# Kernel optimization log

Measured on AMD Instinct MI355X. Metric: run time of the kernel, lower is better.

The kernel has to match this reference:

```python
import jax, jax.numpy as jnp
import numpy as np

SEQ, BATCH, DIM = 2048, 32, 1024


def setup_inputs() -> dict:
    key = jax.random.key(0)
    k1, k2, k3, k4, k5 = jax.random.split(key, 5)
    scale = 1.0 / np.sqrt(DIM)
    return {
        "decoder_hidden": jax.random.normal(k1, (BATCH, 1, DIM), dtype=jnp.float32),
        "encoder_out": jax.random.normal(k2, (SEQ, BATCH, DIM), dtype=jnp.float32),
        "W_enc": jax.random.normal(k3, (DIM, DIM), dtype=jnp.float32) * scale,
        "W_dec": jax.random.normal(k4, (DIM, DIM), dtype=jnp.float32) * scale,
        "V_att": jax.random.normal(k5, (1, DIM), dtype=jnp.float32) * scale,
    }


def reference(decoder_hidden, encoder_out, W_enc, W_dec, V_att):
    # encoder_out: (seq, batch, dim); decoder_hidden: (batch, 1, dim)
    # torch Linear: y = x @ W.T with W of shape (out, in)
    keys = jnp.einsum('sbd,ed->bse', encoder_out, W_enc)      # (batch, seq, dim)
    query = decoder_hidden @ W_dec.T                           # (batch, 1, dim)
    scores = jnp.tanh(keys + query)                            # (batch, seq, dim)
    logits = jnp.einsum('bsd,d->bs', scores, V_att[0])         # (batch, seq)
    alpha = jax.nn.softmax(logits, axis=1)[..., None]          # (batch, seq, 1)
    # context = alpha^T @ encoder_out_permuted -> (batch, 1, dim)
    context = jnp.einsum('bs,sbd->bd', alpha[..., 0], encoder_out)[:, None, :]
    return context, jnp.transpose(alpha, (2, 0, 1))            # (1, batch, seq)
```

## Files before the change

### kernel.cpp

```cpp
#include <hip/hip_runtime.h>
#include <hip/hip_bf16.h>
#include <math.h>

#define SEQ   2048
#define BATCH 32
#define DIM   1024
#define MROWS (SEQ*BATCH)
#define NT2   4
#define NCH   16
#define NKT   32

typedef __attribute__((ext_vector_type(8))) short short8;
typedef __attribute__((ext_vector_type(8))) unsigned short u16x8;
typedef __attribute__((ext_vector_type(4))) float f32x4;

__device__ __forceinline__ unsigned short f2bf(float f) {
  unsigned u = __builtin_bit_cast(unsigned, f);
  u += 0x7FFFu + ((u >> 16) & 1u);
  return (unsigned short)(u >> 16);
}

__device__ __forceinline__ void gl16(const unsigned short* g, unsigned short* l) {
  __builtin_amdgcn_global_load_lds(
      (const __attribute__((address_space(1))) unsigned int*)g,
      (__attribute__((address_space(3))) unsigned int*)l, 16, 0, 0);
}

__global__ __launch_bounds__(256) void conv_bf16_k(const float* __restrict__ src,
                                                   unsigned short* __restrict__ dst) {
  size_t i = ((size_t)blockIdx.x * 256 + threadIdx.x) * 8;
  f32x4 a = __builtin_nontemporal_load(reinterpret_cast<const f32x4*>(src + i));
  f32x4 b = __builtin_nontemporal_load(reinterpret_cast<const f32x4*>(src + i + 4));
  u16x8 o;
  o[0] = f2bf(a[0]); o[1] = f2bf(a[1]); o[2] = f2bf(a[2]); o[3] = f2bf(a[3]);
  o[4] = f2bf(b[0]); o[5] = f2bf(b[1]); o[6] = f2bf(b[2]); o[7] = f2bf(b[3]);
  *reinterpret_cast<u16x8*>(dst + i) = o;
}

__global__ __launch_bounds__(256) void qpart_k(const float* __restrict__ dh,
                                               const float* __restrict__ Wd,
                                               float* __restrict__ qpart) {
  const int bx = blockIdx.x;
  const int eb = bx & 3;
  const int dc = bx >> 2;
  __shared__ float ldh[BATCH][128];
  const int tid = threadIdx.x;
#pragma unroll
  for (int i = 0; i < 4; ++i) {
    int idx = tid + i * 256;
    int bb = idx >> 5, d4 = idx & 31;
    float4 v = *reinterpret_cast<const float4*>(&dh[(size_t)bb * DIM + dc * 128 + d4 * 4]);
    *reinterpret_cast<float4*>(&ldh[bb][d4 * 4]) = v;
  }
  __syncthreads();
  const int e = eb * 256 + tid;
  float acc[BATCH];
#pragma unroll
  for (int b = 0; b < BATCH; ++b) acc[b] = 0.f;
  for (int d4 = 0; d4 < 32; ++d4) {
    float4 w = *reinterpret_cast<const float4*>(&Wd[(size_t)e * DIM + dc * 128 + d4 * 4]);
#pragma unroll
    for (int b = 0; b < BATCH; ++b) {
      float4 h = *reinterpret_cast<const float4*>(&ldh[b][d4 * 4]);
      acc[b] += w.x * h.x + w.y * h.y + w.z * h.z + w.w * h.w;
    }
  }
#pragma unroll
  for (int b = 0; b < BATCH; ++b)
    qpart[((size_t)dc * BATCH + b) * DIM + e] = acc[b];
}

__global__ __launch_bounds__(256) void qred_k(const float* __restrict__ qpart,
                                              float* __restrict__ q) {
  int i = blockIdx.x * 256 + threadIdx.x;
  float s = 0.f;
#pragma unroll
  for (int dc = 0; dc < 8; ++dc) s += qpart[(size_t)dc * 32768 + i];
  q[i] = s;
}

#define BARR  __builtin_amdgcn_s_barrier()
#define VMC(n) asm volatile("s_waitcnt vmcnt(" #n ")" ::: "memory")

#define STAGE_A(t, h) do {                                                        \
    gl16(Abase + (size_t)(gAr + (h) * 64) * 1024 + (t) * 32 + cSt * 8,            \
         (unsigned short*)(arena + (((t) & 1) * 32768) + (h) * 8192) + w * 512);  \
  } while (0)

#define STAGE_B(t, h) do {                                                        \
    gl16(Bbase + (size_t)(gBr + (h) * 32) * 1024 + (t) * 32 + cSt * 8,            \
         (unsigned short*)(arena + (((t) & 1) * 32768) + 16384 + (h) * 8192)      \
             + w * 512);                                                          \
  } while (0)

#define LOAD_A(d, MH) do {                                                        \
    const char* bA_ = arena + (d) * 32768 + (MH) * 8192;                          \
    _Pragma("unroll") for (int i_ = 0; i_ < 4; ++i_) {                            \
      int lrow_ = wr * 64 + i_ * 16 + fr;                                         \
      int lc_ = kq ^ ((lrow_ >> 1) & 3);                                          \
      a[i_] = *(const short8*)(bA_ + lrow_ * 64 + lc_ * 16);                      \
    } } while (0)

#define LOAD_B(SET, d, NH) do {                                                   \
    const char* bB_ = arena + (d) * 32768 + 16384 + (NH) * 8192;                  \
    _Pragma("unroll") for (int j_ = 0; j_ < 2; ++j_) {                            \
      int lrow_ = wc * 32 + j_ * 16 + fr;                                         \
      int lc_ = kq ^ ((lrow_ >> 1) & 3);                                          \
      SET[j_] = *(const short8*)(bB_ + lrow_ * 64 + lc_ * 16);                    \
    } } while (0)

#define QUAD(BSET, MH, NH) do {                                                   \
    __builtin_amdgcn_s_setprio(1);                                                \
    _Pragma("unroll") for (int i_ = 0; i_ < 4; ++i_)                              \
    _Pragma("unroll") for (int j_ = 0; j_ < 2; ++j_)                              \
      acc[(MH) * 4 + i_][(NH) * 2 + j_] =                                         \
          __builtin_amdgcn_mfma_f32_16x16x32_bf16(                                \
              a[i_], BSET[j_], acc[(MH) * 4 + i_][(NH) * 2 + j_], 0, 0, 0);       \
    __builtin_amdgcn_s_setprio(0);                                                \
  } while (0)

__global__ __launch_bounds__(512, 2) void gemm8p(const unsigned short* __restrict__ A,
                                                 const unsigned short* __restrict__ B,
                                                 const float* __restrict__ q,
                                                 const float* __restrict__ V,
                                                 float* __restrict__ lpart) {
  __shared__ __align__(16) char arena[65536];

  const int bid = blockIdx.x;
  const int wg = (bid & 7) * 128 + (bid >> 3);
  const int mt = wg >> 2, nt = wg & 3;
  const int row0 = mt * 256, col0 = nt * 256;
  const int tid = threadIdx.x;
  const int lane = tid & 63, w = tid >> 6;
  const int wr = w >> 2, wc = w & 3;
  const int fr = lane & 15, kq = lane >> 4;

  const int lr0 = tid >> 2;
  const int cSt = (tid & 3) ^ ((lr0 >> 1) & 3);
  const int gAr = (lr0 & 63) + (lr0 >> 6) * 128;
  const int gBr = (lr0 & 31) + (lr0 >> 5) * 64;

  const unsigned short* Abase = A + (size_t)row0 * DIM;
  const unsigned short* Bbase = B + (size_t)col0 * DIM;

  f32x4 acc[8][4];
#pragma unroll
  for (int i = 0; i < 8; ++i)
#pragma unroll
    for (int j = 0; j < 4; ++j) acc[i][j] = (f32x4)(0.f);

  short8 a[4];
  short8 b0[2], b1[2];

  STAGE_A(0, 0); STAGE_B(0, 0); STAGE_A(0, 1); STAGE_B(0, 1);
  STAGE_A(1, 0); STAGE_B(1, 0);
  VMC(2);
  BARR;

#pragma unroll 1
  for (int t2 = 0; t2 < NKT; t2 += 2) {
    const bool last = (t2 == NKT - 2);
    LOAD_A(0, 0); LOAD_B(b0, 0, 0); LOAD_B(b1, 0, 1);
    STAGE_A(t2 + 1, 1); STAGE_B(t2 + 1, 1);
    BARR; QUAD(b0, 0, 0); QUAD(b1, 0, 1); BARR;
    LOAD_A(0, 1);
    if (!last) { STAGE_A(t2 + 2, 0); STAGE_B(t2 + 2, 0); VMC(2); } else { VMC(0); }
    BARR; QUAD(b0, 1, 0); QUAD(b1, 1, 1); BARR;
    LOAD_A(1, 0); LOAD_B(b0, 1, 0); LOAD_B(b1, 1, 1);
    if (!last) { STAGE_A(t2 + 2, 1); STAGE_B(t2 + 2, 1); }
    BARR; QUAD(b0, 0, 0); QUAD(b1, 0, 1); BARR;
    LOAD_A(1, 1);
    if (!last) { STAGE_A(t2 + 3, 0); STAGE_B(t2 + 3, 0); VMC(2); }
    BARR; QUAD(b0, 1, 0); QUAD(b1, 1, 1); BARR;
  }

  __syncthreads();
  float* qld = (float*)arena;
  float* vld = (float*)(arena + 33280);
  float* red = (float*)(arena + 34304);
#pragma unroll
  for (int i = 0; i < 4; ++i) {
    int id = i * 512 + tid;
    int bb = id >> 6, e4 = id & 63;
    float4 v = *(const float4*)&q[(size_t)bb * DIM + col0 + e4 * 4];
    *(float4*)&qld[bb * 260 + e4 * 4] = v;
  }
  if (tid < 64) *(float4*)&vld[tid * 4] = *(const float4*)&V[col0 + tid * 4];
  __syncthreads();

#pragma unroll
  for (int mf = 0; mf < 8; ++mf) {
#pragma unroll
    for (int reg = 0; reg < 4; ++reg) {
      const int m_loc = wr * 128 + mf * 16 + kq * 4 + reg;
      const int bb = m_loc & 31;
      float val = 0.f;
#pragma unroll
      for (int nf = 0; nf < 4; ++nf) {
        const int el = wc * 64 + nf * 16 + fr;
        float x = acc[mf][nf][reg] + qld[bb * 260 + el];
        float g = __expf(2.f * x);
        float tnh = 1.f - 2.f * __builtin_amdgcn_rcpf(g + 1.f);
        val += tnh * vld[el];
      }
      val += __shfl_xor(val, 1); val += __shfl_xor(val, 2);
      val += __shfl_xor(val, 4); val += __shfl_xor(val, 8);
      if (fr == 0) red[wc * 256 + m_loc] = val;
    }
  }
  __syncthreads();
  if (tid < 256) {
    float s = red[tid] + red[256 + tid] + red[512 + tid] + red[768 + tid];
    lpart[(size_t)(row0 + tid) * NT2 + nt] = s;
  }
}

__global__ __launch_bounds__(256) void softmax_k(const float* __restrict__ lpart,
                                                 float* __restrict__ alpha) {
  const int b = blockIdx.x;
  __shared__ float lv[SEQ];
  __shared__ float sred[4];
  const int tid = threadIdx.x;
  float mx = -1e30f;
  for (int s = tid; s < SEQ; s += 256) {
    const float* p = &lpart[(size_t)(s * BATCH + b) * NT2];
    float v = p[0] + p[1] + p[2] + p[3];
    lv[s] = v;
    mx = fmaxf(mx, v);
  }
#pragma unroll
  for (int off = 32; off >= 1; off >>= 1) mx = fmaxf(mx, __shfl_xor(mx, off));
  if ((tid & 63) == 0) sred[tid >> 6] = mx;
  __syncthreads();
  mx = fmaxf(fmaxf(sred[0], sred[1]), fmaxf(sred[2], sred[3]));
  __syncthreads();
  float sm = 0.f;
  for (int s = tid; s < SEQ; s += 256) {
    float e = expf(lv[s] - mx);
    lv[s] = e;
    sm += e;
  }
#pragma unroll
  for (int off = 32; off >= 1; off >>= 1) sm += __shfl_xor(sm, off);
  if ((tid & 63) == 0) sred[tid >> 6] = sm;
  __syncthreads();
  const float inv = 1.f / (sred[0] + sred[1] + sred[2] + sred[3]);
  for (int s = tid; s < SEQ; s += 256)
    alpha[(size_t)b * SEQ + s] = lv[s] * inv;
}

__global__ __launch_bounds__(256) void ctx_part_k(const unsigned short* __restrict__ encbf,
                                                  const float* __restrict__ alpha,
                                                  float* __restrict__ cpart) {
  const int blk = blockIdx.x;
  const int b = blk & 31;
  const int ch = blk >> 5;
  const int tid = threadIdx.x;
  const int g = tid >> 7;
  const int d0 = (tid & 127) * 8;
  const int s0 = ch * (SEQ / NCH);
  float acc8[8];
#pragma unroll
  for (int k = 0; k < 8; ++k) acc8[k] = 0.f;
#pragma unroll 4
  for (int i = 0; i < SEQ / NCH; i += 2) {
    const int s = s0 + i + g;
    const float a = alpha[(size_t)b * SEQ + s];
    u16x8 v = *reinterpret_cast<const u16x8*>(&encbf[((size_t)s * BATCH + b) * DIM + d0]);
#pragma unroll
    for (int k = 0; k < 8; ++k) {
      float f = __builtin_bit_cast(float, (unsigned)v[k] << 16);
      acc8[k] += a * f;
    }
  }
  size_t o = ((size_t)(ch * 2 + g) * BATCH + b) * DIM + d0;
  float4 lo = {acc8[0], acc8[1], acc8[2], acc8[3]};
  float4 hi = {acc8[4], acc8[5], acc8[6], acc8[7]};
  *(float4*)&cpart[o] = lo;
  *(float4*)&cpart[o + 4] = hi;
}

__global__ __launch_bounds__(256) void ctxred_k(const float* __restrict__ cpart,
                                                float* __restrict__ out) {
  int i = blockIdx.x * 256 + threadIdx.x;
  float s = 0.f;
#pragma unroll
  for (int ch = 0; ch < 32; ++ch) s += cpart[(size_t)ch * 32768 + i];
  out[i] = s;
}

extern "C" void kernel_launch(void* const* d_in, const int* in_sizes, int n_in,
                              void* d_out, int out_size, void* d_ws, size_t ws_size,
                              hipStream_t stream) {
  const float* dh   = (const float*)d_in[0];
  const float* enc  = (const float*)d_in[1];
  const float* Wenc = (const float*)d_in[2];
  const float* Wdec = (const float*)d_in[3];
  const float* Vatt = (const float*)d_in[4];
  float* out = (float*)d_out;

  float* ws = (float*)d_ws;
  float* q      = ws;
  float* qpart  = ws + 32768;
  float* lpart  = ws + 294912;
  float* cpart  = ws + 557056;
  unsigned short* Wbf   = (unsigned short*)(ws + 1605632);
  unsigned short* encbf = (unsigned short*)(ws + 2129920);

  conv_bf16_k<<<dim3(512),   dim3(256), 0, stream>>>(Wenc, Wbf);
  qpart_k    <<<dim3(32),    dim3(256), 0, stream>>>(dh, Wdec, qpart);
  qred_k     <<<dim3(128),   dim3(256), 0, stream>>>(qpart, q);
  conv_bf16_k<<<dim3(32768), dim3(256), 0, stream>>>(enc, encbf);
  gemm8p     <<<dim3(1024),  dim3(512), 0, stream>>>(encbf, Wbf, q, Vatt, lpart);
  softmax_k  <<<dim3(BATCH),     dim3(256), 0, stream>>>(lpart, out + 32768);
  ctx_part_k <<<dim3(BATCH*NCH), dim3(256), 0, stream>>>(encbf, out + 32768, cpart);
  ctxred_k   <<<dim3(128),       dim3(256), 0, stream>>>(cpart, out);
}
```

Baseline: 280.9 us.

## Retile attention GEMM to 16 waves with 64-wide K tiles

The fused score GEMM now runs 1024-thread blocks of 16 waves, each owning a 64x64 sub-tile of the 256x256 output instead of 128x64. The K step doubles to 64, and the LDS arena grows to 128 KB to hold double-buffered A and B tiles, with an XOR swizzle over 8 chunks. The goal is to halve the number of K iterations and barriers and to put more waves on each CU to hide latency. In exchange, the large LDS footprint likely limits each CU to one block. Staging the next tile into a half-buffer while other waves may still be reading it adds a possible race.

```diff
diff --git a/kernel.cpp b/kernel.cpp
--- a/kernel.cpp
+++ b/kernel.cpp
@@ -8,7 +8,7 @@
 #define MROWS (SEQ*BATCH)
 #define NT2   4
 #define NCH   16
-#define NKT   32
+#define NKT   16
 
 typedef __attribute__((ext_vector_type(8))) short short8;
 typedef __attribute__((ext_vector_type(8))) unsigned short u16x8;
@@ -83,48 +83,47 @@
 #define VMC(n) asm volatile("s_waitcnt vmcnt(" #n ")" ::: "memory")
 
 #define STAGE_A(t, h) do {                                                        \
-    gl16(Abase + (size_t)(gAr + (h) * 64) * 1024 + (t) * 32 + cSt * 8,            \
-         (unsigned short*)(arena + (((t) & 1) * 32768) + (h) * 8192) + w * 512);  \
+    gl16(Abase + (size_t)(lr0 + (h) * 128) * 1024 + (t) * 64 + cSt * 8,           \
+         (unsigned short*)(arena + (((t) & 1) * 65536) + (h) * 16384) + w * 512); \
   } while (0)
 
 #define STAGE_B(t, h) do {                                                        \
-    gl16(Bbase + (size_t)(gBr + (h) * 32) * 1024 + (t) * 32 + cSt * 8,            \
-         (unsigned short*)(arena + (((t) & 1) * 32768) + 16384 + (h) * 8192)      \
+    gl16(Bbase + (size_t)(lr0 + (h) * 128) * 1024 + (t) * 64 + cSt * 8,           \
+         (unsigned short*)(arena + (((t) & 1) * 65536) + 32768 + (h) * 16384)     \
              + w * 512);                                                          \
   } while (0)
 
-#define LOAD_A(d, MH) do {                                                        \
-    const char* bA_ = arena + (d) * 32768 + (MH) * 8192;                          \
+#define LOAD_A(d, ks) do {                                                        \
+    const char* bA_ = arena + (d) * 65536 + (wr >> 1) * 16384;                    \
     _Pragma("unroll") for (int i_ = 0; i_ < 4; ++i_) {                            \
-      int lrow_ = wr * 64 + i_ * 16 + fr;                                         \
-      int lc_ = kq ^ ((lrow_ >> 1) & 3);                                          \
-      a[i_] = *(const short8*)(bA_ + lrow_ * 64 + lc_ * 16);                      \
+      int row_ = (wr & 1) * 64 + i_ * 16 + fr;                                    \
+      int lc_ = ((ks) * 4 + kq) ^ (fr & 7);                                       \
+      a[i_] = *(const short8*)(bA_ + row_ * 128 + lc_ * 16);                      \
     } } while (0)
 
-#define LOAD_B(SET, d, NH) do {                                                   \
-    const char* bB_ = arena + (d) * 32768 + 16384 + (NH) * 8192;                  \
-    _Pragma("unroll") for (int j_ = 0; j_ < 2; ++j_) {                            \
-      int lrow_ = wc * 32 + j_ * 16 + fr;                                         \
-      int lc_ = kq ^ ((lrow_ >> 1) & 3);                                          \
-      SET[j_] = *(const short8*)(bB_ + lrow_ * 64 + lc_ * 16);                    \
+#define LOAD_B(d, ks) do {                                                        \
+    const char* bB_ = arena + (d) * 65536 + 32768 + (wc >> 1) * 16384;            \
+    _Pragma("unroll") for (int j_ = 0; j_ < 4; ++j_) {                            \
+      int row_ = (wc & 1) * 64 + j_ * 16 + fr;                                    \
+      int lc_ = ((ks) * 4 + kq) ^ (fr & 7);                                       \
+      b[j_] = *(const short8*)(bB_ + row_ * 128 + lc_ * 16);                      \
     } } while (0)
 
-#define QUAD(BSET, MH, NH) do {                                                   \
+#define QUAD() do {                                                               \
     __builtin_amdgcn_s_setprio(1);                                                \
     _Pragma("unroll") for (int i_ = 0; i_ < 4; ++i_)                              \
-    _Pragma("unroll") for (int j_ = 0; j_ < 2; ++j_)                              \
-      acc[(MH) * 4 + i_][(NH) * 2 + j_] =                                         \
-          __builtin_amdgcn_mfma_f32_16x16x32_bf16(                                \
-              a[i_], BSET[j_], acc[(MH) * 4 + i_][(NH) * 2 + j_], 0, 0, 0);       \
+    _Pragma("unroll") for (int j_ = 0; j_ < 4; ++j_)                              \
+      acc[i_][j_] = __builtin_amdgcn_mfma_f32_16x16x32_bf16(                      \
+          a[i_], b[j_], acc[i_][j_], 0, 0, 0);                                    \
     __builtin_amdgcn_s_setprio(0);                                                \
   } while (0)
 
-__global__ __launch_bounds__(512, 2) void gemm8p(const unsigned short* __restrict__ A,
-                                                 const unsigned short* __restrict__ B,
-                                                 const float* __restrict__ q,
-                                                 const float* __restrict__ V,
-                                                 float* __restrict__ lpart) {
-  __shared__ __align__(16) char arena[65536];
+__global__ __launch_bounds__(1024, 4) void gemm8p(const unsigned short* __restrict__ A,
+                                                  const unsigned short* __restrict__ B,
+                                                  const float* __restrict__ q,
+                                                  const float* __restrict__ V,
+                                                  float* __restrict__ lpart) {
+  __shared__ __align__(16) char arena[131072];
 
   const int bid = blockIdx.x;
   const int wg = (bid & 7) * 128 + (bid >> 3);
@@ -135,22 +134,19 @@
   const int wr = w >> 2, wc = w & 3;
   const int fr = lane & 15, kq = lane >> 4;
 
-  const int lr0 = tid >> 2;
-  const int cSt = (tid & 3) ^ ((lr0 >> 1) & 3);
-  const int gAr = (lr0 & 63) + (lr0 >> 6) * 128;
-  const int gBr = (lr0 & 31) + (lr0 >> 5) * 64;
+  const int lr0 = tid >> 3;
+  const int cSt = (tid & 7) ^ (lr0 & 7);
 
   const unsigned short* Abase = A + (size_t)row0 * DIM;
   const unsigned short* Bbase = B + (size_t)col0 * DIM;
 
-  f32x4 acc[8][4];
-#pragma unroll
-  for (int i = 0; i < 8; ++i)
+  f32x4 acc[4][4];
+#pragma unroll
+  for (int i = 0; i < 4; ++i)
 #pragma unroll
     for (int j = 0; j < 4; ++j) acc[i][j] = (f32x4)(0.f);
 
-  short8 a[4];
-  short8 b0[2], b1[2];
+  short8 a[4], b[4];
 
   STAGE_A(0, 0); STAGE_B(0, 0); STAGE_A(0, 1); STAGE_B(0, 1);
   STAGE_A(1, 0); STAGE_B(1, 0);
@@ -160,18 +156,18 @@
 #pragma unroll 1
   for (int t2 = 0; t2 < NKT; t2 += 2) {
     const bool last = (t2 == NKT - 2);
-    LOAD_A(0, 0); LOAD_B(b0, 0, 0); LOAD_B(b1, 0, 1);
+    LOAD_A(0, 0); LOAD_B(0, 0);
     STAGE_A(t2 + 1, 1); STAGE_B(t2 + 1, 1);
-    BARR; QUAD(b0, 0, 0); QUAD(b1, 0, 1); BARR;
-    LOAD_A(0, 1);
+    BARR; QUAD(); BARR;
+    LOAD_A(0, 1); LOAD_B(0, 1);
     if (!last) { STAGE_A(t2 + 2, 0); STAGE_B(t2 + 2, 0); VMC(2); } else { VMC(0); }
-    BARR; QUAD(b0, 1, 0); QUAD(b1, 1, 1); BARR;
-    LOAD_A(1, 0); LOAD_B(b0, 1, 0); LOAD_B(b1, 1, 1);
+    BARR; QUAD(); BARR;
+    LOAD_A(1, 0); LOAD_B(1, 0);
     if (!last) { STAGE_A(t2 + 2, 1); STAGE_B(t2 + 2, 1); }
-    BARR; QUAD(b0, 0, 0); QUAD(b1, 0, 1); BARR;
-    LOAD_A(1, 1);
+    BARR; QUAD(); BARR;
+    LOAD_A(1, 1); LOAD_B(1, 1);
     if (!last) { STAGE_A(t2 + 3, 0); STAGE_B(t2 + 3, 0); VMC(2); }
-    BARR; QUAD(b0, 1, 0); QUAD(b1, 1, 1); BARR;
+    BARR; QUAD(); BARR;
   }
 
   __syncthreads();
@@ -179,8 +175,8 @@
   float* vld = (float*)(arena + 33280);
   float* red = (float*)(arena + 34304);
 #pragma unroll
-  for (int i = 0; i < 4; ++i) {
-    int id = i * 512 + tid;
+  for (int i = 0; i < 2; ++i) {
+    int id = i * 1024 + tid;
     int bb = id >> 6, e4 = id & 63;
     float4 v = *(const float4*)&q[(size_t)bb * DIM + col0 + e4 * 4];
     *(float4*)&qld[bb * 260 + e4 * 4] = v;
@@ -189,10 +185,10 @@
   __syncthreads();
 
 #pragma unroll
-  for (int mf = 0; mf < 8; ++mf) {
+  for (int mf = 0; mf < 4; ++mf) {
 #pragma unroll
     for (int reg = 0; reg < 4; ++reg) {
-      const int m_loc = wr * 128 + mf * 16 + kq * 4 + reg;
+      const int m_loc = wr * 64 + mf * 16 + kq * 4 + reg;
       const int bb = m_loc & 31;
       float val = 0.f;
 #pragma unroll
@@ -311,7 +307,7 @@
   qpart_k    <<<dim3(32),    dim3(256), 0, stream>>>(dh, Wdec, qpart);
   qred_k     <<<dim3(128),   dim3(256), 0, stream>>>(qpart, q);
   conv_bf16_k<<<dim3(32768), dim3(256), 0, stream>>>(enc, encbf);
-  gemm8p     <<<dim3(1024),  dim3(512), 0, stream>>>(encbf, Wbf, q, Vatt, lpart);
+  gemm8p     <<<dim3(1024),  dim3(1024), 0, stream>>>(encbf, Wbf, q, Vatt, lpart);
   softmax_k  <<<dim3(BATCH),     dim3(256), 0, stream>>>(lpart, out + 32768);
   ctx_part_k <<<dim3(BATCH*NCH), dim3(256), 0, stream>>>(encbf, out + 32768, cpart);
   ctxred_k   <<<dim3(128),       dim3(256), 0, stream>>>(cpart, out);
```

After: 268.1 us. -4.6%, faster.
